# Optimization experiments

Hardware: AMD Instinct MI355X
Metric: run time of the kernel (lower is better)

Reference implementation:

```python
import jax, jax.numpy as jnp
import numpy as np

NUM_HEADS = 16


def setup_inputs() -> dict:
    key = jax.random.key(0)
    k1, k2, k3, k4 = jax.random.split(key, 4)
    in_dim, out_dim = 1024, 1024
    x = jax.random.normal(k1, (4, 2048, in_dim), dtype=jnp.float32)
    # nn.Linear weights stored as [out, in]; we keep that convention.
    s = 1.0 / np.sqrt(in_dim)
    Wq = jax.random.uniform(k2, (out_dim, in_dim), jnp.float32, -s, s)
    Wk = jax.random.uniform(k3, (out_dim, in_dim), jnp.float32, -s, s)
    Wv = jax.random.uniform(k4, (out_dim, in_dim), jnp.float32, -s, s)
    return {"x": x, "Wq": Wq, "Wk": Wk, "Wv": Wv}


def reference(x, Wq, Wk, Wv):
    b, n, _ = x.shape
    out_dim = Wq.shape[0]
    h = NUM_HEADS
    d = out_dim // h  # head_dim

    def split_heads(t):  # [b,n,out] -> [b,h,n,d]
        return t.reshape(b, n, h, d).transpose(0, 2, 1, 3)

    q = split_heads(x @ Wq.T)
    k = split_heads(x @ Wk.T)
    v = split_heads(x @ Wv.T)

    scores = jnp.einsum("bhqd,bhkd->bhqk", q, k) / jnp.sqrt(jnp.float32(d))
    causal = jnp.tril(jnp.ones((n, n), dtype=bool))
    scores = jnp.where(causal, scores, -jnp.inf)
    attn = jax.nn.softmax(scores, axis=-1)
    out = jnp.einsum("bhqk,bhkd->bhqd", attn, v)
    return out.transpose(0, 2, 1, 3).reshape(b, n, out_dim)
```

## Files before the change

kernel.cpp:

```cpp
#include <hip/hip_runtime.h>

typedef __attribute__((ext_vector_type(8))) short short8;
typedef __attribute__((ext_vector_type(4))) short short4v;
typedef __attribute__((ext_vector_type(4))) float floatx4;
typedef __attribute__((ext_vector_type(16))) float floatx16;
typedef __attribute__((ext_vector_type(2))) int iv2;

#define GLOBAL_AS __attribute__((address_space(1)))
#define LDS_AS __attribute__((address_space(3)))

__device__ __forceinline__ short f2bs(float f) {
    union { float f; unsigned u; } v; v.f = f;
    unsigned r = v.u + 0x7fffu + ((v.u >> 16) & 1u);
    return (short)(r >> 16);
}

#if __has_builtin(__builtin_amdgcn_cvt_pk_bf16_f32)
typedef __attribute__((ext_vector_type(2))) __bf16 bf16x2;
__device__ __forceinline__ unsigned pk2(float a, float b) {
    union { bf16x2 v; unsigned u; } u;
    u.v = __builtin_amdgcn_cvt_pk_bf16_f32(a, b);
    return u.u;
}
#else
__device__ __forceinline__ unsigned pk2(float a, float b) {
    union { float f; unsigned u; } x, y; x.f = a; y.f = b;
    return ((y.u + 0x8000u) & 0xffff0000u) | ((x.u + 0x8000u) >> 16);
}
#endif

__global__ __launch_bounds__(256) void cast_all(const float* __restrict__ x,
                                                const float* __restrict__ Wq,
                                                const float* __restrict__ Wk,
                                                const float* __restrict__ Wv,
                                                short* __restrict__ xb,
                                                short* __restrict__ wb) {
    int b = blockIdx.x;
    int t = threadIdx.x;
    const float* src;
    short* dst;
    int idx;
    if (b < 8192) {
        src = x; dst = xb; idx = b * 1024 + t * 4;
    } else {
        int r = b - 8192;
        int wz = r >> 10;
        src = (wz == 0) ? Wq : (wz == 1) ? Wk : Wv;
        dst = wb + wz * (1 << 20);
        idx = (r & 1023) * 1024 + t * 4;
    }
    float4 v = *(const float4*)(src + idx);
    short4v o;
    o.x = f2bs(v.x); o.y = f2bs(v.y); o.z = f2bs(v.z); o.w = f2bs(v.w);
    *(short4v*)(dst + idx) = o;
}

__global__ __launch_bounds__(256) void qkv_gemm(const short* __restrict__ xb,
                                                const short* __restrict__ wb,
                                                short* __restrict__ qout,
                                                short* __restrict__ kout,
                                                short* __restrict__ vtout) {
    __shared__ short As[2][128 * 64];
    __shared__ short Bs[2][128 * 64];
    const int K = 1024;
    int tid = threadIdx.x;
    int lane = tid & 63;
    int wid = tid >> 6;
    int quad = lane >> 4;
    int l16 = lane & 15;
    int wm = (wid >> 1) * 64;
    int wn = (wid & 1) * 64;
    int bm = blockIdx.x * 128;
    int bn = blockIdx.y * 128;
    const short* W = wb + (size_t)blockIdx.z * K * 1024;

    floatx4 acc[4][4];
#pragma unroll
    for (int i = 0; i < 4; i++)
#pragma unroll
        for (int j = 0; j < 4; j++) acc[i][j] = (floatx4){0.f, 0.f, 0.f, 0.f};

    int srow = tid >> 3;
    int ssw = ((tid & 7) ^ (srow & 7)) * 8;

#define STAGE_AB(cb, kk) do { \
    _Pragma("unroll") for (int l = 0; l < 4; l++) { \
        const short* g = xb + (size_t)(bm + srow + l * 32) * K + (kk) + ssw; \
        __builtin_amdgcn_global_load_lds((const GLOBAL_AS void*)g, \
            (LDS_AS void*)(&As[cb][0] + tid * 8 + l * 2048), 16, 0, 0); \
    } \
    _Pragma("unroll") for (int l = 0; l < 4; l++) { \
        const short* g = W + (size_t)(bn + srow + l * 32) * K + (kk) + ssw; \
        __builtin_amdgcn_global_load_lds((const GLOBAL_AS void*)g, \
            (LDS_AS void*)(&Bs[cb][0] + tid * 8 + l * 2048), 16, 0, 0); \
    } \
} while (0)

    STAGE_AB(0, 0);

    for (int T = 0; T < 16; T++) {
        int cur = T & 1;
        __builtin_amdgcn_sched_barrier(0);
        __builtin_amdgcn_s_barrier();
        __builtin_amdgcn_sched_barrier(0);
        if (T < 15) {
            STAGE_AB(cur ^ 1, (T + 1) * 64);
            asm volatile("s_waitcnt vmcnt(8)" ::: "memory");
        } else {
            asm volatile("s_waitcnt vmcnt(0)" ::: "memory");
        }
        __builtin_amdgcn_sched_barrier(0);
        __builtin_amdgcn_s_barrier();
        __builtin_amdgcn_sched_barrier(0);

        const short* Ac = &As[cur][0];
        const short* Bc = &Bs[cur][0];
#pragma unroll
        for (int s = 0; s < 2; s++) {
            int slot = ((s * 4 + quad) ^ (l16 & 7)) * 8;
            short8 af[4], bf[4];
#pragma unroll
            for (int i = 0; i < 4; i++)
                af[i] = *(const short8*)(Ac + (wm + i * 16 + l16) * 64 + slot);
#pragma unroll
            for (int j = 0; j < 4; j++)
                bf[j] = *(const short8*)(Bc + (wn + j * 16 + l16) * 64 + slot);
#pragma unroll
            for (int i = 0; i < 4; i++)
#pragma unroll
                for (int j = 0; j < 4; j++)
                    acc[i][j] = __builtin_amdgcn_mfma_f32_16x16x32_bf16(af[i], bf[j], acc[i][j], 0, 0, 0);
        }
    }
#undef STAGE_AB

    if (blockIdx.z == 2) {
#pragma unroll
        for (int i = 0; i < 4; i++) {
#pragma unroll
            for (int j = 0; j < 4; j++) {
                int m = bm + wm + i * 16 + quad * 4;
                int c = bn + wn + j * 16 + l16;
                int b = m >> 11, nn = m & 2047, h = c >> 6, dd = c & 63;
                short4v pk;
                pk.x = f2bs(acc[i][j][0]);
                pk.y = f2bs(acc[i][j][1]);
                pk.z = f2bs(acc[i][j][2]);
                pk.w = f2bs(acc[i][j][3]);
                *(short4v*)(vtout + ((size_t)(b * 16 + h) * 64 + dd) * 2048 + nn) = pk;
            }
        }
    } else {
        short* dst = (blockIdx.z == 0) ? qout : kout;
        float qs = (blockIdx.z == 0) ? 0.180336881f : 1.0f;
#pragma unroll
        for (int i = 0; i < 4; i++) {
#pragma unroll
            for (int j = 0; j < 4; j++) {
#pragma unroll
                for (int r = 0; r < 4; r++) {
                    int m = bm + wm + i * 16 + quad * 4 + r;
                    int c = bn + wn + j * 16 + l16;
                    dst[((size_t)((m >> 11) * 16 + (c >> 6)) * 2048 + (m & 2047)) * 64 + (c & 63)] =
                        f2bs(acc[i][j][r] * qs);
                }
            }
        }
    }
}

__global__ __launch_bounds__(256, 2) void attn(const short* __restrict__ q,
                                               const short* __restrict__ k,
                                               const short* __restrict__ vt,
                                               float* __restrict__ out) {
    __shared__ short Ks[2][128 * 64];
    __shared__ short Vs[2][64 * 128];

    int tid = threadIdx.x;
    int lane = tid & 63;
    int wid = tid >> 6;
    int l32 = lane & 31;
    int half = lane >> 5;

    int flat = blockIdx.x;
    int xcd = flat & 7;
    int slot = flat >> 3;
    int bh = xcd * 8 + (slot >> 3);
    int qx = slot & 7;
    int b = bh >> 4, h = bh & 15;

    const short* qp = q + (size_t)(b * 16 + h) * 2048 * 64;
    const short* kp = k + (size_t)(b * 16 + h) * 2048 * 64;
    const short* vp = vt + (size_t)(b * 16 + h) * 64 * 2048;

    int krow = tid >> 3;
    int ksw = ((tid & 7) ^ (krow & 7)) * 8;
    int vd = tid >> 4;
    int vc = tid & 15;
    int vsw = ((vc & 8) | ((vc ^ vd) & 7)) * 8;

#define BARRIER() asm volatile("s_barrier" ::: "memory")
#define STAGE_KV(cb, kvb) do { \
    _Pragma("unroll") for (int l = 0; l < 4; l++) { \
        const short* g = kp + (size_t)((kvb) + krow + l * 32) * 64 + ksw; \
        __builtin_amdgcn_global_load_lds((const GLOBAL_AS void*)g, \
            (LDS_AS void*)(&Ks[cb][0] + tid * 8 + l * 2048), 16, 0, 0); \
    } \
    _Pragma("unroll") for (int l = 0; l < 4; l++) { \
        const short* g = vp + (size_t)(vd + l * 16) * 2048 + (kvb) + vsw; \
        __builtin_amdgcn_global_load_lds((const GLOBAL_AS void*)g, \
            (LDS_AS void*)(&Vs[cb][0] + tid * 8 + l * 2048), 16, 0, 0); \
    } \
} while (0)

#define STREAM_TILE(qf, qlane, oacc, rs, isdiag) do { \
    floatx16 sacc[4]; \
    _Pragma("unroll") for (int kb = 0; kb < 4; kb++) \
    _Pragma("unroll") for (int e = 0; e < 16; e++) sacc[kb][e] = 0.f; \
    __builtin_amdgcn_s_setprio(1); \
    _Pragma("unroll") for (int s = 0; s < 4; s++) { \
        _Pragma("unroll") for (int kb = 0; kb < 4; kb++) { \
            int key = kb * 32 + l32; \
            int c = s * 2 + half; \
            short8 kf = *(const short8*)(Kc + key * 64 + ((c ^ (key & 7)) * 8)); \
            sacc[kb] = __builtin_amdgcn_mfma_f32_32x32x16_bf16(kf, qf[s], sacc[kb], 0, 0, 0); \
        } \
    } \
    __builtin_amdgcn_s_setprio(0); \
    unsigned W0[4][4], W1[4][4]; \
    _Pragma("unroll") for (int kb = 0; kb < 4; kb++) { \
        _Pragma("unroll") for (int e = 0; e < 16; e++) { \
            float p = __builtin_amdgcn_exp2f(sacc[kb][e]); \
            if (isdiag) { \
                int key = kvb + kb * 32 + (e & 3) + 8 * (e >> 2) + 4 * half; \
                p = (key > (qlane)) ? 0.f : p; \
            } \
            sacc[kb][e] = p; \
            rs += p; \
        } \
        _Pragma("unroll") for (int g = 0; g < 4; g++) { \
            W0[kb][g] = pk2(sacc[kb][4 * g + 0], sacc[kb][4 * g + 1]); \
            W1[kb][g] = pk2(sacc[kb][4 * g + 2], sacc[kb][4 * g + 3]); \
        } \
    } \
    __builtin_amdgcn_s_setprio(1); \
    _Pragma("unroll") for (int s = 0; s < 8; s++) { \
        int kb = s >> 1; \
        int g0 = (s & 1) * 2; \
        int g1 = g0 + 1; \
        iv2 r0 = __builtin_amdgcn_permlane32_swap(W0[kb][g0], W0[kb][g1], false, false); \
        iv2 r1 = __builtin_amdgcn_permlane32_swap(W1[kb][g0], W1[kb][g1], false, false); \
        union { int4 v; short8 s8; } pu; \
        pu.v.x = r0.x; pu.v.y = r1.x; pu.v.z = r0.y; pu.v.w = r1.y; \
        short8 pf = pu.s8; \
        _Pragma("unroll") for (int nt = 0; nt < 2; nt++) { \
            int d = nt * 32 + l32; \
            int c = s * 2 + half; \
            int sl = (c & 8) | ((c ^ (d & 7)) & 7); \
            short8 vf = *(const short8*)(Vc + d * 128 + sl * 8); \
            oacc[nt] = __builtin_amdgcn_mfma_f32_32x32x16_bf16(pf, vf, oacc[nt], 0, 0, 0); \
        } \
    } \
    __builtin_amdgcn_s_setprio(0); \
} while (0)

#define EPILOG(rs, oacc, qrow_w) do { \
    float tot = (rs) + __shfl_xor((rs), 32); \
    float inv = 1.0f / tot; \
    float invr[16]; \
    _Pragma("unroll") for (int e = 0; e < 16; e++) \
        invr[e] = __shfl(inv, (e & 3) + 8 * (e >> 2) + 4 * half); \
    _Pragma("unroll") for (int nt = 0; nt < 2; nt++) { \
        _Pragma("unroll") for (int e = 0; e < 16; e++) { \
            int r = (e & 3) + 8 * (e >> 2) + 4 * half; \
            int nn = (qrow_w) + r; \
            out[((size_t)b * 2048 + nn) * 1024 + h * 64 + nt * 32 + l32] = oacc[nt][e] * invr[e]; \
        } \
    } \
} while (0)

    int qA = qx;
    int qB = 15 - qx;
    int NT = qB + 1;

    int qrowA = qA * 128 + wid * 32;
    int qrowB = qB * 128 + wid * 32;
    int qlaneA = qrowA + l32;
    int qlaneB = qrowB + l32;

    short8 qfA[4], qfB[4];
#pragma unroll
    for (int s = 0; s < 4; s++) {
        qfA[s] = *(const short8*)(qp + (size_t)qlaneA * 64 + s * 16 + half * 8);
        qfB[s] = *(const short8*)(qp + (size_t)qlaneB * 64 + s * 16 + half * 8);
    }

    floatx16 oaccA[2], oaccB[2];
#pragma unroll
    for (int nt = 0; nt < 2; nt++)
#pragma unroll
        for (int e = 0; e < 16; e++) { oaccA[nt][e] = 0.f; oaccB[nt][e] = 0.f; }
    float rsA = 0.f, rsB = 0.f;

    STAGE_KV(0, 0);

    for (int t = 0; t < NT; t++) {
        int cur = t & 1;
        int kvb = t * 128;

        BARRIER();
        if (t + 1 < NT) {
            STAGE_KV(cur ^ 1, kvb + 128);
            asm volatile("s_waitcnt vmcnt(8)" ::: "memory");
        } else {
            asm volatile("s_waitcnt vmcnt(0)" ::: "memory");
        }
        BARRIER();

        const short* Kc = &Ks[cur][0];
        const short* Vc = &Vs[cur][0];

        if (t <= qA) {
            bool dA = (t == qA);
            STREAM_TILE(qfA, qlaneA, oaccA, rsA, dA);
        }
        {
            bool dB = (t == NT - 1);
            STREAM_TILE(qfB, qlaneB, oaccB, rsB, dB);
        }
    }

    EPILOG(rsA, oaccA, qrowA);
    EPILOG(rsB, oaccB, qrowB);

#undef STREAM_TILE
#undef EPILOG
#undef STAGE_KV
#undef BARRIER
}

extern "C" void kernel_launch(void* const* d_in, const int* in_sizes, int n_in,
                              void* d_out, int out_size, void* d_ws, size_t ws_size,
                              hipStream_t stream) {
    const float* x = (const float*)d_in[0];
    const float* Wq = (const float*)d_in[1];
    const float* Wk = (const float*)d_in[2];
    const float* Wv = (const float*)d_in[3];
    float* out = (float*)d_out;
    char* ws = (char*)d_ws;

    short* xb = (short*)ws;
    short* wb = (short*)(ws + (16u << 20));
    short* qb = (short*)(ws + (22u << 20));
    short* kb = (short*)(ws + (38u << 20));
    short* vtb = (short*)(ws + (54u << 20));

    cast_all<<<8192 + 3 * 1024, 256, 0, stream>>>(x, Wq, Wk, Wv, xb, wb);
    qkv_gemm<<<dim3(64, 8, 3), 256, 0, stream>>>(xb, wb, qb, kb, vtb);
    attn<<<512, 256, 0, stream>>>(qb, kb, vtb, out);
}
```

Measured before the change: 209.4 us.

## Shrink KV tiles to 64 keys with 4-stage ring buffer and single barrier

The attention kernel now streams K/V in 64-key tiles through a 4-deep LDS ring, prefetching two tiles ahead and using one barrier per iteration instead of two. The diagonal mask check is now computed per warp from its query row, so warps whose rows lie entirely past the tile skip masking work. The aim is deeper load/compute overlap and less barrier overhead. In exchange there are twice as many iterations, with smaller MFMA batches per barrier and more loop overhead.

Result: no change. 213.0 us (+1.7%).

```diff
diff --git a/kernel.cpp b/kernel.cpp
--- a/kernel.cpp
+++ b/kernel.cpp
@@ -173,8 +173,8 @@
                                                const short* __restrict__ k,
                                                const short* __restrict__ vt,
                                                float* __restrict__ out) {
-    __shared__ short Ks[2][128 * 64];
-    __shared__ short Vs[2][64 * 128];
+    __shared__ short Ks[4][64 * 64];
+    __shared__ short Vs[4][64 * 64];
 
     int tid = threadIdx.x;
     int lane = tid & 63;
@@ -193,33 +193,30 @@
     const short* kp = k + (size_t)(b * 16 + h) * 2048 * 64;
     const short* vp = vt + (size_t)(b * 16 + h) * 64 * 2048;
 
-    int krow = tid >> 3;
-    int ksw = ((tid & 7) ^ (krow & 7)) * 8;
-    int vd = tid >> 4;
-    int vc = tid & 15;
-    int vsw = ((vc & 8) | ((vc ^ vd) & 7)) * 8;
+    int srow = tid >> 3;
+    int ssw = ((tid & 7) ^ (srow & 7)) * 8;
 
 #define BARRIER() asm volatile("s_barrier" ::: "memory")
 #define STAGE_KV(cb, kvb) do { \
-    _Pragma("unroll") for (int l = 0; l < 4; l++) { \
-        const short* g = kp + (size_t)((kvb) + krow + l * 32) * 64 + ksw; \
+    _Pragma("unroll") for (int l = 0; l < 2; l++) { \
+        const short* g = kp + (size_t)((kvb) + srow + l * 32) * 64 + ssw; \
         __builtin_amdgcn_global_load_lds((const GLOBAL_AS void*)g, \
             (LDS_AS void*)(&Ks[cb][0] + tid * 8 + l * 2048), 16, 0, 0); \
     } \
-    _Pragma("unroll") for (int l = 0; l < 4; l++) { \
-        const short* g = vp + (size_t)(vd + l * 16) * 2048 + (kvb) + vsw; \
+    _Pragma("unroll") for (int l = 0; l < 2; l++) { \
+        const short* g = vp + (size_t)(srow + l * 32) * 2048 + (kvb) + ssw; \
         __builtin_amdgcn_global_load_lds((const GLOBAL_AS void*)g, \
             (LDS_AS void*)(&Vs[cb][0] + tid * 8 + l * 2048), 16, 0, 0); \
     } \
 } while (0)
 
 #define STREAM_TILE(qf, qlane, oacc, rs, isdiag) do { \
-    floatx16 sacc[4]; \
-    _Pragma("unroll") for (int kb = 0; kb < 4; kb++) \
+    floatx16 sacc[2]; \
+    _Pragma("unroll") for (int kb = 0; kb < 2; kb++) \
     _Pragma("unroll") for (int e = 0; e < 16; e++) sacc[kb][e] = 0.f; \
     __builtin_amdgcn_s_setprio(1); \
     _Pragma("unroll") for (int s = 0; s < 4; s++) { \
-        _Pragma("unroll") for (int kb = 0; kb < 4; kb++) { \
+        _Pragma("unroll") for (int kb = 0; kb < 2; kb++) { \
             int key = kb * 32 + l32; \
             int c = s * 2 + half; \
             short8 kf = *(const short8*)(Kc + key * 64 + ((c ^ (key & 7)) * 8)); \
@@ -227,8 +224,8 @@
         } \
     } \
     __builtin_amdgcn_s_setprio(0); \
-    unsigned W0[4][4], W1[4][4]; \
-    _Pragma("unroll") for (int kb = 0; kb < 4; kb++) { \
+    unsigned W0[2][4], W1[2][4]; \
+    _Pragma("unroll") for (int kb = 0; kb < 2; kb++) { \
         _Pragma("unroll") for (int e = 0; e < 16; e++) { \
             float p = __builtin_amdgcn_exp2f(sacc[kb][e]); \
             if (isdiag) { \
@@ -244,7 +241,7 @@
         } \
     } \
     __builtin_amdgcn_s_setprio(1); \
-    _Pragma("unroll") for (int s = 0; s < 8; s++) { \
+    _Pragma("unroll") for (int s = 0; s < 4; s++) { \
         int kb = s >> 1; \
         int g0 = (s & 1) * 2; \
         int g1 = g0 + 1; \
@@ -256,8 +253,7 @@
         _Pragma("unroll") for (int nt = 0; nt < 2; nt++) { \
             int d = nt * 32 + l32; \
             int c = s * 2 + half; \
-            int sl = (c & 8) | ((c ^ (d & 7)) & 7); \
-            short8 vf = *(const short8*)(Vc + d * 128 + sl * 8); \
+            short8 vf = *(const short8*)(Vc + d * 64 + ((c ^ (d & 7)) * 8)); \
             oacc[nt] = __builtin_amdgcn_mfma_f32_32x32x16_bf16(pf, vf, oacc[nt], 0, 0, 0); \
         } \
     } \
@@ -281,7 +277,8 @@
 
     int qA = qx;
     int qB = 15 - qx;
-    int NT = qB + 1;
+    int NT = 2 * qB + 2;
+    int lastA = 2 * qA + 1;
 
     int qrowA = qA * 128 + wid * 32;
     int qrowB = qB * 128 + wid * 32;
@@ -303,29 +300,29 @@
     float rsA = 0.f, rsB = 0.f;
 
     STAGE_KV(0, 0);
+    STAGE_KV(1, 64);
 
     for (int t = 0; t < NT; t++) {
-        int cur = t & 1;
-        int kvb = t * 128;
-
-        BARRIER();
+        int kvb = t * 64;
+
         if (t + 1 < NT) {
-            STAGE_KV(cur ^ 1, kvb + 128);
-            asm volatile("s_waitcnt vmcnt(8)" ::: "memory");
+            asm volatile("s_waitcnt vmcnt(4)" ::: "memory");
         } else {
             asm volatile("s_waitcnt vmcnt(0)" ::: "memory");
         }
         BARRIER();
 
-        const short* Kc = &Ks[cur][0];
-        const short* Vc = &Vs[cur][0];
-
-        if (t <= qA) {
-            bool dA = (t == qA);
+        if (t + 2 < NT) STAGE_KV((t + 2) & 3, kvb + 128);
+
+        const short* Kc = &Ks[t & 3][0];
+        const short* Vc = &Vs[t & 3][0];
+
+        if (t <= lastA) {
+            bool dA = (kvb + 63 > qrowA);
             STREAM_TILE(qfA, qlaneA, oaccA, rsA, dA);
         }
         {
-            bool dB = (t == NT - 1);
+            bool dB = (kvb + 63 > qrowB);
             STREAM_TILE(qfB, qlaneB, oaccB, rsB, dB);
         }
     }
```
